# Kernel tuning notes

Hardware: AMD Instinct MI355X
Metric: run time of the kernel (lower is better)

The kernel has to match this reference:

```python
import jax, jax.numpy as jnp
import numpy as np
from jax import lax

FAULT_RATE = 0.1


def _quant_inject(key, x, num_faults):
    # scale/zero-point quantization to [0,255] (matches compute_scale_zero_point)
    mn, mx = x.min(), x.max()
    scale = (mx - mn) / 255.0
    zp = jnp.clip(-mn / scale, 0.0, 255.0)
    q = jnp.clip(jnp.round(zp + x / scale), 0.0, 255.0)
    if num_faults > 0:
        # vectorized equivalent of the serial fault loop: pick unique indices,
        # each consumes a random 1..8 fault budget; faulted bytes are zeroed
        # (the original loop sets tensor_bits = 0).
        n = q.size
        m = min(num_faults, n)  # each index consumes >= 1 fault
        k1, k2 = jax.random.split(key)
        cand = jax.random.permutation(k1, n)[:m]  # without replacement
        sizes = jax.random.randint(k2, (m,), 1, 9)
        prefix = jnp.cumsum(sizes) - sizes  # budget consumed before each pick
        keep = prefix < num_faults
        qf = q.reshape(-1)
        qf = qf.at[cand].set(jnp.where(keep, jnp.zeros((), q.dtype), qf[cand]))
        q = qf.reshape(q.shape)
    return scale * (q - zp)


def _conv(x, w, b):
    y = lax.conv_general_dilated(x, w, (1, 1), 'VALID',
                                 dimension_numbers=('NCHW', 'OIHW', 'NCHW'))
    return y + b[None, :, None, None]


def _maxpool(x):
    return lax.reduce_window(x, -np.inf, lax.max, (1, 1, 2, 2), (1, 1, 2, 2), 'VALID')


def _fault_schedule(total_activation_count):
    total_faults = int(total_activation_count * 8 * FAULT_RATE)
    rng = np.random.default_rng(0)
    return [int(v) for v in rng.multinomial(total_faults, np.ones(4) / 4)]


def _forward(x, conv1_w, conv1_b, conv2_w, conv2_b, fc_w, fc_b,
             fc1_w, fc1_b, fc2_w, fc2_b, fpl):
    ks = jax.random.split(jax.random.key(42), 11)
    x = _conv(x, conv1_w, conv1_b)
    x = _quant_inject(ks[0], x, 0)
    x = jax.nn.relu(x)
    x = _quant_inject(ks[1], x, fpl[0])
    x = _maxpool(x)
    x = _quant_inject(ks[2], x, 0)
    x = _conv(x, conv2_w, conv2_b)
    x = _quant_inject(ks[3], x, 0)
    x = jax.nn.relu(x)
    x = _quant_inject(ks[4], x, fpl[1])
    x = _maxpool(x)
    x = _quant_inject(ks[5], x, 0)
    x = x.reshape(x.shape[0], -1)  # [B, 400]
    x = x @ fc_w.T + fc_b
    x = _quant_inject(ks[6], x, 0)
    x = jax.nn.relu(x)
    x = _quant_inject(ks[7], x, fpl[2])
    x = x @ fc1_w.T + fc1_b
    x = _quant_inject(ks[8], x, 0)
    x = jax.nn.relu(x)
    x = _quant_inject(ks[9], x, fpl[3])
    x = x @ fc2_w.T + fc2_b
    x = _quant_inject(ks[10], x, 0)
    return jax.nn.log_softmax(x, axis=1)


def setup_inputs() -> dict:
    key = jax.random.key(0)
    ks = jax.random.split(key, 11)
    B = 8192
    return {
        'x': jax.random.normal(ks[0], (B, 1, 32, 32), jnp.float32),
        'conv1_w': jax.random.normal(ks[1], (6, 1, 5, 5), jnp.float32) * 0.2,
        'conv1_b': jax.random.normal(ks[2], (6,), jnp.float32) * 0.1,
        'conv2_w': jax.random.normal(ks[3], (16, 6, 5, 5), jnp.float32) * 0.08,
        'conv2_b': jax.random.normal(ks[4], (16,), jnp.float32) * 0.1,
        'fc_w': jax.random.normal(ks[5], (120, 400), jnp.float32) * 0.05,
        'fc_b': jax.random.normal(ks[6], (120,), jnp.float32) * 0.1,
        'fc1_w': jax.random.normal(ks[7], (84, 120), jnp.float32) * 0.09,
        'fc1_b': jax.random.normal(ks[8], (84,), jnp.float32) * 0.1,
        'fc2_w': jax.random.normal(ks[9], (10, 84), jnp.float32) * 0.1,
        'fc2_b': jax.random.normal(ks[10], (10,), jnp.float32) * 0.1,
        'total_activation_count': 833024,
    }


def reference(x, conv1_w, conv1_b, conv2_w, conv2_b, fc_w, fc_b,
              fc1_w, fc1_b, fc2_w, fc2_b, total_activation_count):
    fpl = _fault_schedule(total_activation_count)
    return _forward(x, conv1_w, conv1_b, conv2_w, conv2_b, fc_w, fc_b,
                    fc1_w, fc1_b, fc2_w, fc2_b, fpl)
```

## Files before the change

### kernel.cpp

```cpp
#include <hip/hip_runtime.h>
#include <cstdint>
#include <cstring>
#include <cmath>
#include <cstdlib>
#include <vector>
#include <thread>
#include <mutex>
#include <algorithm>

#define JAX_PARTITIONABLE 1


static inline uint32_t rotl32(uint32_t v, int d) { return (v << d) | (v >> (32 - d)); }

static inline void tf2x32(uint32_t k0, uint32_t k1, uint32_t c0, uint32_t c1,
                          uint32_t& o0, uint32_t& o1) {
  uint32_t ks0 = k0, ks1 = k1, ks2 = k0 ^ k1 ^ 0x1BD11BDAu;
  uint32_t ks[3] = {ks0, ks1, ks2};
  uint32_t x0 = c0 + ks0, x1 = c1 + ks1;
  static const int R[2][4] = {{13, 15, 26, 6}, {17, 29, 16, 24}};
  for (int g = 0; g < 5; g++) {
    const int* r = R[g & 1];
    for (int q = 0; q < 4; q++) { x0 += x1; x1 = rotl32(x1, r[q]); x1 ^= x0; }
    x0 += ks[(g + 1) % 3];
    x1 += ks[(g + 2) % 3] + (uint32_t)(g + 1);
  }
  o0 = x0; o1 = x1;
}

static void jax_split(const uint32_t key[2], int num, uint32_t (*out)[2]) {
#if JAX_PARTITIONABLE
  for (int i = 0; i < num; i++)
    tf2x32(key[0], key[1], 0u, (uint32_t)i, out[i][0], out[i][1]);
#else
  std::vector<uint32_t> o(2 * (size_t)num);
  for (int i = 0; i < num; i++) {
    uint32_t a, b;
    tf2x32(key[0], key[1], (uint32_t)i, (uint32_t)(num + i), a, b);
    o[i] = a; o[num + i] = b;
  }
  for (int i = 0; i < num; i++) { out[i][0] = o[2 * i]; out[i][1] = o[2 * i + 1]; }
#endif
}

static inline uint32_t jax_bits32_at(const uint32_t key[2], uint64_t n_total, uint64_t i) {
#if JAX_PARTITIONABLE
  uint32_t b0, b1;
  tf2x32(key[0], key[1], (uint32_t)(i >> 32), (uint32_t)i, b0, b1);
  return b0 ^ b1;
#else
  uint64_t half = (n_total + 1) / 2;
  uint64_t pi = (i < half) ? i : (i - half);
  uint32_t c1 = (half + pi < n_total) ? (uint32_t)(half + pi) : 0u;
  uint32_t b0, b1;
  tf2x32(key[0], key[1], (uint32_t)pi, c1, b0, b1);
  return (i < half) ? b0 : b1;
#endif
}

static void seedseq_zero_state(uint64_t out[4]) {
  const uint32_t INIT_A = 0x43b0d7e5u, MULT_A = 0x931e8875u;
  const uint32_t INIT_B = 0x8b51f9ddu, MULT_B = 0x58f38dedu;
  uint32_t pool[4];
  uint32_t hc = INIT_A;
  auto hashmix = [&](uint32_t v) -> uint32_t {
    v ^= hc; hc *= MULT_A; v *= hc; v ^= v >> 16; return v;
  };
  auto mixf = [](uint32_t x, uint32_t y) -> uint32_t {
    uint32_t r = x * 0xca01f9ddu - y * 0x4973f715u;
    r ^= r >> 16; return r;
  };
  uint32_t entropy0 = 0u;
  for (int i = 0; i < 4; i++) pool[i] = hashmix(i < 1 ? entropy0 : 0u);
  for (int s = 0; s < 4; s++)
    for (int d = 0; d < 4; d++)
      if (s != d) pool[d] = mixf(pool[d], hashmix(pool[s]));
  uint32_t st[8];
  uint32_t hc2 = INIT_B;
  int cyc = 0;
  for (int i = 0; i < 8; i++) {
    uint32_t v = pool[cyc]; cyc = (cyc + 1) & 3;
    v ^= hc2; hc2 *= MULT_B; v *= hc2; v ^= v >> 16;
    st[i] = v;
  }
  for (int k = 0; k < 4; k++)
    out[k] = (uint64_t)st[2 * k] | ((uint64_t)st[2 * k + 1] << 32);
}

struct PCG64 {
  __uint128_t state, inc;
  explicit PCG64(const uint64_t s[4]) {
    __uint128_t initstate = (((__uint128_t)s[0]) << 64) | s[1];
    __uint128_t initseq = (((__uint128_t)s[2]) << 64) | s[3];
    state = 0; inc = (initseq << 1) | 1;
    step(); state += initstate; step();
  }
  void step() {
    const __uint128_t MUL =
        (((__uint128_t)0x2360ed051fc65da4ULL) << 64) | 0x4385df649fccf645ULL;
    state = state * MUL + inc;
  }
  uint64_t next64() {
    step();
    uint64_t hi = (uint64_t)(state >> 64), lo = (uint64_t)state;
    uint64_t x = hi ^ lo;
    unsigned rot = (unsigned)(state >> 122);
    return (x >> rot) | (x << ((64u - rot) & 63u));
  }
  double nextd() { return (double)(next64() >> 11) * (1.0 / 9007199254740992.0); }
};

static int64_t binomial_inversion(PCG64& st, int64_t n, double p) {
  double q = 1.0 - p;
  double qn = std::exp(n * std::log(q));
  double np_ = n * p;
  int64_t bound = (int64_t)std::min((double)n, np_ + 10.0 * std::sqrt(np_ * q + 1));
  int64_t X = 0;
  double px = qn;
  double U = st.nextd();
  while (U > px) {
    X++;
    if (X > bound) { X = 0; px = qn; U = st.nextd(); }
    else { U -= px; px = ((n - X + 1) * p * px) / (X * q); }
  }
  return X;
}

static int64_t random_binomial_btpe(PCG64& st, int64_t n, double p) {
  double r, q, fm, p1, xm, xl, xr, c, laml, lamr, p2, p3, p4;
  double a, u, v, s, F, rho, t, A, nrq, x1, x2, f1, f2, z, z2, w, w2, x;
  int64_t m, y, k, i;
  r = std::min(p, 1.0 - p);
  q = 1.0 - r;
  fm = n * r + r;
  m = (int64_t)std::floor(fm);
  p1 = std::floor(2.195 * std::sqrt(n * r * q) - 4.6 * q) + 0.5;
  xm = m + 0.5;
  xl = xm - p1;
  xr = xm + p1;
  c = 0.134 + 20.5 / (15.3 + m);
  a = (fm - xl) / (fm - xl * r);
  laml = a * (1.0 + a / 2.0);
  a = (xr - fm) / (xr * q);
  lamr = a * (1.0 + a / 2.0);
  p2 = p1 * (1.0 + 2.0 * c);
  p3 = p2 + c / laml;
  p4 = p3 + c / lamr;

Step10:
  nrq = n * r * q;
  u = st.nextd() * p4;
  v = st.nextd();
  if (u > p1) goto Step20;
  y = (int64_t)std::floor(xm - p1 * v + u);
  goto Step60;
Step20:
  if (u > p2) goto Step30;
  x = xl + (u - p1) / c;
  v = v * c + 1.0 - std::fabs(m - x + 0.5) / p1;
  if (v > 1.0) goto Step10;
  y = (int64_t)std::floor(x);
  goto Step50;
Step30:
  if (u > p3) goto Step40;
  y = (int64_t)std::floor(xl + std::log(v) / laml);
  if ((y < 0) || (v == 0.0)) goto Step10;
  v = v * (u - p2) * laml;
  goto Step50;
Step40:
  y = (int64_t)std::floor(xr - std::log(v) / lamr);
  if ((y > n) || (v == 0.0)) goto Step10;
  v = v * (u - p3) * lamr;
  goto Step50;
Step50:
  k = (y > m) ? (y - m) : (m - y);
  if ((k > 20) && (k < (nrq / 2.0 - 1))) goto Step52;
  s = r / q;
  a = s * (n + 1);
  F = 1.0;
  if (m < y) { for (i = m + 1; i <= y; i++) F *= (a / i - s); }
  else if (m > y) { for (i = y + 1; i <= m; i++) F /= (a / i - s); }
  if (v > F) goto Step10;
  goto Step60;
Step52:
  rho = ((double)k / nrq) * ((k * (k / 3.0 + 0.625) + 0.16666666666666666) / nrq + 0.5);
  t = -((double)k) * k / (2 * nrq);
  A = std::log(v);
  if (A < (t - rho)) goto Step60;
  if (A > (t + rho)) goto Step10;
  x1 = (double)(y + 1);
  f1 = (double)(m + 1);
  z = (double)(n + 1 - m);
  w = (double)(n - y + 1);
  x2 = x1 * x1; f2 = f1 * f1; z2 = z * z; w2 = w * w;
  if (A > (xm * std::log(f1 / x1) + (n - m + 0.5) * std::log(z / w) +
           (y - m) * std::log(w * r / (x1 * q)) +
           (13680. - (462. - (132. - (99. - 140. / f2) / f2) / f2) / f2) / f1 / 166320. +
           (13680. - (462. - (132. - (99. - 140. / z2) / z2) / z2) / z2) / z / 166320. +
           (13680. - (462. - (132. - (99. - 140. / x2) / x2) / x2) / x2) / x1 / 166320. +
           (13680. - (462. - (132. - (99. - 140. / w2) / w2) / w2) / w2) / w / 166320.)) {
    goto Step10;
  }
Step60:
  if (p > 0.5) y = n - y;
  return y;
}

static int64_t random_binomial(PCG64& st, double p, int64_t n) {
  if (n == 0 || p == 0.0) return 0;
  if (p <= 0.5) {
    if (p * n <= 30.0) return binomial_inversion(st, n, p);
    return random_binomial_btpe(st, n, p);
  } else {
    double q = 1.0 - p;
    if (q * n <= 30.0) return n - binomial_inversion(st, n, q);
    return n - random_binomial_btpe(st, n, q);
  }
}

static void np_multinomial4(int64_t n, int64_t out[4]) {
  uint64_t ss[4];
  seedseq_zero_state(ss);
  PCG64 st(ss);
  double pix[4] = {0.25, 0.25, 0.25, 0.25};
  double remaining_p = 1.0;
  int64_t dn = n;
  out[0] = out[1] = out[2] = out[3] = 0;
  for (int j = 0; j < 3; j++) {
    out[j] = random_binomial(st, pix[j] / remaining_p, dn);
    dn -= out[j];
    if (dn <= 0) break;
    remaining_p -= pix[j];
  }
  if (dn > 0) out[3] = dn;
}

template <typename F>
static void pfor(size_t n, int T, const F& f) {
  if (n == 0) return;
  size_t chunk = (n + (size_t)T - 1) / (size_t)T;
  std::vector<std::thread> ths;
  for (int t = 0; t < T; t++) {
    size_t lo = (size_t)t * chunk;
    if (lo >= n) break;
    size_t hi = std::min(n, lo + chunk);
    ths.emplace_back([&f, lo, hi, t]() { f(lo, hi, t); });
  }
  for (auto& th : ths) th.join();
}

static void radix_pass16(const uint32_t* kin, const uint32_t* vin, uint32_t* kout,
                         uint32_t* vout, size_t n, int shift, int T,
                         std::vector<uint32_t>& hist) {
  const size_t BN = 65536;
  hist.assign((size_t)T * BN, 0u);
  pfor(n, T, [&](size_t lo, size_t hi, int t) {
    uint32_t* h = &hist[(size_t)t * BN];
    for (size_t i = lo; i < hi; i++) h[(kin[i] >> shift) & 0xFFFFu]++;
  });
  uint32_t sum = 0;
  for (size_t d = 0; d < BN; d++)
    for (int t = 0; t < T; t++) {
      uint32_t& hc = hist[(size_t)t * BN + d];
      uint32_t cnt = hc; hc = sum; sum += cnt;
    }
  pfor(n, T, [&](size_t lo, size_t hi, int t) {
    uint32_t* h = &hist[(size_t)t * BN];
    for (size_t i = lo; i < hi; i++) {
      uint32_t d = (kin[i] >> shift) & 0xFFFFu;
      uint32_t pos = h[d]++;
      kout[pos] = kin[i]; vout[pos] = vin[i];
    }
  });
}

static void shuffle_prefix(const uint32_t key[2], uint64_t n, uint32_t J,
                           uint32_t* out, int T) {
  if (J == 0) return;
  double nn = (double)(n < 1 ? 1 : n);
  int rounds = (int)std::ceil(3.0 * std::log(nn) / std::log(4294967295.0));
  size_t N = (size_t)n;
  std::vector<uint32_t> kbuf(N), vbuf(N), kt(N), vt(N);
  std::vector<uint32_t> hist;
  pfor(N, T, [&](size_t lo, size_t hi, int) {
    for (size_t i = lo; i < hi; i++) vbuf[i] = (uint32_t)i;
  });
  uint32_t cur[2] = {key[0], key[1]};
  for (int rd = 0; rd < rounds; rd++) {
    uint32_t ch[2][2];
    jax_split(cur, 2, ch);
    cur[0] = ch[0][0]; cur[1] = ch[0][1];
    uint32_t sk[2] = {ch[1][0], ch[1][1]};
#if JAX_PARTITIONABLE
    pfor(N, T, [&](size_t lo, size_t hi, int) {
      for (size_t i = lo; i < hi; i++) {
        uint32_t b0, b1;
        tf2x32(sk[0], sk[1], (uint32_t)(i >> 32), (uint32_t)i, b0, b1);
        kbuf[i] = b0 ^ b1;
      }
    });
#else
    {
      size_t half = (N + 1) / 2;
      pfor(half, T, [&](size_t lo, size_t hi, int) {
        for (size_t i = lo; i < hi; i++) {
          uint32_t c1v = (half + i < N) ? (uint32_t)(half + i) : 0u;
          uint32_t b0, b1;
          tf2x32(sk[0], sk[1], (uint32_t)i, c1v, b0, b1);
          kbuf[i] = b0;
          if (half + i < N) kbuf[half + i] = b1;
        }
      });
    }
#endif
    radix_pass16(kbuf.data(), vbuf.data(), kt.data(), vt.data(), N, 0, T, hist);
    radix_pass16(kt.data(), vt.data(), kbuf.data(), vbuf.data(), N, 16, T, hist);
  }
  for (uint32_t j = 0; j < J; j++) out[j] = vbuf[j];
  std::sort(out, out + J);
}


static uint32_t h_faults[4 * 65536];
static uint32_t h_blob[64 + 5 * 65536];
static int h_J[4] = {0, 0, 0, 0};
static int h_off[4] = {0, 0, 0, 0};
static int h_tot = 0;
static int h_nfw = 0;
static uint64_t h_tables_B = 0;

static void compute_fault_tables(uint64_t B, int Jout[4]) {
  int T = (int)std::thread::hardware_concurrency();
  if (T < 1) T = 1;
  if (T > 48) T = 48;
  int64_t fpl[4];
  np_multinomial4((int64_t)(833024ull * 8ull / 10ull), fpl);
  uint32_t k42[2] = {0u, 42u};
  uint32_t ks[11][2];
  jax_split(k42, 11, ks);
  const int kidx[4] = {1, 4, 7, 9};
  const uint64_t ns[4] = {B * 4704u, B * 1600u, B * 120u, B * 84u};
  for (int L = 0; L < 4; L++) {
    uint32_t ch[2][2];
    jax_split(ks[kidx[L]], 2, ch);
    uint32_t rc[2][2];
    jax_split(ch[1], 2, rc);
    int64_t nf = fpl[L];
    uint64_t m = ((uint64_t)nf < ns[L]) ? (uint64_t)nf : ns[L];
    int64_t csum = 0;
    uint32_t J = 0;
    for (uint64_t j = 0; j < m; j++) {
      if (csum >= nf) break;
      J++;
      csum += 1 + (int64_t)(jax_bits32_at(rc[1], m, j) & 7u);
    }
    if (J > 65536u) J = 65536u;
    shuffle_prefix(ch[0], ns[L], J, &h_faults[(size_t)L * 65536], T);
    Jout[L] = (int)J;
  }
  memset(h_blob, 0, 256);
  for (int s = 0; s < 11; s++) { h_blob[2 * s] = 0xFFFFFFFFu; h_blob[2 * s + 1] = 0u; }
  int tot = 0;
  for (int L = 0; L < 4; L++) {
    h_off[L] = tot;
    memcpy(h_blob + 64 + tot, h_faults + (size_t)L * 65536, (size_t)Jout[L] * 4);
    tot += Jout[L];
  }
  h_tot = tot;
  {
    std::vector<uint32_t> wv;
    wv.reserve(Jout[0]);
    for (int j = 0; j < Jout[0]; j++) {
      uint32_t e = h_faults[j];
      uint32_t im = e / 4704u, rem = e - im * 4704u;
      uint32_t c = rem / 784u, r2 = rem - c * 784u;
      uint32_t rr = r2 / 28u, cc = r2 - rr * 28u;
      wv.push_back(im * 1176u + c * 196u + (rr >> 1) * 14u + (cc >> 1));
    }
    std::sort(wv.begin(), wv.end());
    wv.erase(std::unique(wv.begin(), wv.end()), wv.end());
    h_nfw = (int)std::min<size_t>(wv.size(), 65536);
    memcpy(h_blob + 64 + tot, wv.data(), (size_t)h_nfw * 4);
  }
}

namespace {
struct FaultTableInit {
  FaultTableInit() {
    compute_fault_tables(8192ull, h_J);
    h_tables_B = 8192ull;
  }
};
FaultTableInit g_fault_table_init;
std::mutex g_table_mu;
}


#define INF_F __builtin_inff()

__device__ __forceinline__ uint32_t f_to_mono(float f) {
  uint32_t u = __float_as_uint(f);
  return (u & 0x80000000u) ? ~u : (u | 0x80000000u);
}
__device__ __forceinline__ float mono_to_f(uint32_t m) {
  uint32_t u = (m & 0x80000000u) ? (m & 0x7FFFFFFFu) : ~m;
  return __uint_as_float(u);
}

struct QP { float scale; float zp; };

__device__ __forceinline__ QP qp_make(float mn, float mx) {
  QP p;
  p.scale = (mx - mn) / 255.0f;
  p.zp = fminf(fmaxf((-mn) / p.scale, 0.0f), 255.0f);
  return p;
}
__device__ __forceinline__ QP qp_load(const uint32_t* stats, int s) {
  return qp_make(mono_to_f(stats[2 * s + 0]), mono_to_f(stats[2 * s + 1]));
}
__device__ __forceinline__ float quant_apply(float x, QP p) {
  float q = rintf(p.zp + x / p.scale);
  q = fminf(fmaxf(q, 0.0f), 255.0f);
  return p.scale * (q - p.zp);
}
__device__ __forceinline__ float quant_zero(QP p) { return p.scale * (0.0f - p.zp); }
__device__ __forceinline__ int q_idx(float x, QP p) {
  float q = rintf(p.zp + x / p.scale);
  q = fminf(fmaxf(q, 0.0f), 255.0f);
  return (int)q;
}

__device__ __forceinline__ QP qp_derive_relu(const uint32_t* stats, int s, QP qa) {
  float mn = mono_to_f(stats[2 * s + 0]);
  float mx = mono_to_f(stats[2 * s + 1]);
  float dmn = fmaxf(quant_apply(mn, qa), 0.0f);
  float dmx = fmaxf(quant_apply(mx, qa), 0.0f);
  return qp_make(dmn, dmx);
}

__device__ __forceinline__ void block_minmax(float lmn, float lmx, uint32_t* mn_slot,
                                             uint32_t* mx_slot) {
  for (int off = 32; off > 0; off >>= 1) {
    lmn = fminf(lmn, __shfl_down(lmn, off, 64));
    lmx = fmaxf(lmx, __shfl_down(lmx, off, 64));
  }
  __shared__ float wmn[16], wmx[16];
  int wid = threadIdx.x >> 6, lane = threadIdx.x & 63;
  int nw = (blockDim.x + 63) >> 6;
  if (lane == 0) { wmn[wid] = lmn; wmx[wid] = lmx; }
  __syncthreads();
  if (threadIdx.x == 0) {
    float m0 = wmn[0], m1 = wmx[0];
    for (int i = 1; i < nw; i++) { m0 = fminf(m0, wmn[i]); m1 = fmaxf(m1, wmx[i]); }
    atomicMin(mn_slot, f_to_mono(m0));
    atomicMax(mx_slot, f_to_mono(m1));
  }
}

__device__ __forceinline__ int lowb(const uint32_t* a, int n, uint32_t v) {
  int lo = 0, hi = n;
  while (lo < hi) {
    int mid = (lo + hi) >> 1;
    if (a[mid] < v) lo = mid + 1; else hi = mid;
  }
  return lo;
}


template <int IMG>
__device__ __forceinline__ void stage_img(const float* __restrict__ x, float* s_img,
                                          int ib0, int B) {
  for (int i = threadIdx.x; i < IMG * 256; i += 256) {
    int im = i >> 8, k = i & 255;
    if (ib0 + im < B) {
      float4 v = ((const float4*)(x + (size_t)(ib0 + im) * 1024))[k];
      int row = k >> 3, c4 = k & 7;
      ((float4*)s_img)[im * 320 + row * 10 + c4] = v;
    }
  }
}

__device__ __forceinline__ void stage_w1(const float* __restrict__ w, float* s_w) {
  if (threadIdx.x < 168) {
    int c = threadIdx.x / 28, f = threadIdx.x - c * 28;
    s_w[threadIdx.x] = (f < 25) ? w[c * 25 + f] : 0.0f;
  }
}

template <int O>
__device__ __forceinline__ void conv1_rowpair(const float* __restrict__ img, int r0,
                                              int colbase, const float* wr,
                                              float acc0[14], float acc1[14]) {
#pragma unroll
  for (int ir = 0; ir < 6; ir++) {
    float f[20];
    const float* rp = img + (r0 + ir) * 40 + colbase;
#pragma unroll
    for (int k = 0; k < 5; k++) *(float4*)&f[4 * k] = *(const float4*)&rp[4 * k];
    if (ir < 5) {
#pragma unroll
      for (int j = 0; j < 5; j++)
#pragma unroll
        for (int cc = 0; cc < 14; cc++)
          acc0[cc] = fmaf(f[O + cc + j], wr[ir * 5 + j], acc0[cc]);
    }
    if (ir >= 1) {
#pragma unroll
      for (int j = 0; j < 5; j++)
#pragma unroll
        for (int cc = 0; cc < 14; cc++)
          acc1[cc] = fmaf(f[O + cc + j], wr[(ir - 1) * 5 + j], acc1[cc]);
    }
  }
}

__global__ __launch_bounds__(256) void k_conv1_mat(const float* __restrict__ x,
    const float* __restrict__ w, const float* __restrict__ b,
    float* __restrict__ wmax, float* __restrict__ side,
    const uint32_t* __restrict__ fw, int nfw_g,
    uint32_t* __restrict__ stats, int B) {
  __shared__ __align__(16) float s_img[4 * 1280];
  __shared__ __align__(16) float s_w[168];
  __shared__ float s_b[8];
  __shared__ uint32_t s_fw[64];
  __shared__ int s_flo, s_fn;
  int ib0 = blockIdx.x * 4;
  stage_img<4>(x, s_img, ib0, B);
  stage_w1(w, s_w);
  if (threadIdx.x < 6) s_b[threadIdx.x] = b[threadIdx.x];
  if (threadIdx.x == 0) {
    uint32_t w0 = (uint32_t)ib0 * 1176u;
    uint32_t w1 = (uint32_t)(ib0 + 4) * 1176u;
    int lo = lowb(fw, nfw_g, w0);
    s_flo = lo; s_fn = lowb(fw, nfw_g, w1) - lo;
  }
  __syncthreads();
  int fn = s_fn, flo = s_flo;
  for (int i = threadIdx.x; i < fn && i < 64; i += 256) s_fw[i] = fw[flo + i];
  __syncthreads();
  const uint32_t* fwa = (fn <= 64) ? s_fw : (fw + flo);

  float lmn = INF_F, lmx = -INF_F;
#pragma unroll 1
  for (int task = threadIdx.x; task < 4 * 168; task += 256) {
    int im = task / 168, rem = task - im * 168;
    if (ib0 + im >= B) continue;
    int c = rem / 28, r2 = rem - c * 28, pr = r2 >> 1, h = r2 & 1;
    float wr[25];
#pragma unroll
    for (int k = 0; k < 25; k++) wr[k] = s_w[c * 28 + k];
    float bias = s_b[c];
    float acc0[14], acc1[14];
#pragma unroll
    for (int cc = 0; cc < 14; cc++) { acc0[cc] = bias; acc1[cc] = bias; }
    const float* img = &s_img[im * 1280];
    if (h == 0) conv1_rowpair<0>(img, 2 * pr, 0, wr, acc0, acc1);
    else        conv1_rowpair<2>(img, 2 * pr, 12, wr, acc0, acc1);
    uint32_t wid0 = (uint32_t)(ib0 + im) * 1176u + (uint32_t)(c * 196 + pr * 14 + h * 7);
    float* dst = wmax + wid0;
#pragma unroll
    for (int k = 0; k < 7; k++) {
      float wm = fmaxf(fmaxf(acc0[2 * k], acc0[2 * k + 1]),
                       fmaxf(acc1[2 * k], acc1[2 * k + 1]));
      dst[k] = wm;
    }
    if (fn > 0) {
      int a = lowb(fwa, fn, wid0);
      while (a < fn) {
        uint32_t wg = fwa[a];
        if (wg >= wid0 + 7u) break;
#pragma unroll
        for (int k = 0; k < 7; k++) {
          if ((int)(wg - wid0) == k) {
            float4 sv;
            sv.x = acc0[2 * k]; sv.y = acc0[2 * k + 1];
            sv.z = acc1[2 * k]; sv.w = acc1[2 * k + 1];
            *(float4*)&side[4 * (flo + a)] = sv;
          }
        }
        a++;
      }
    }
#pragma unroll
    for (int cc = 0; cc < 14; cc++) {
      lmn = fminf(lmn, fminf(acc0[cc], acc1[cc]));
      lmx = fmaxf(lmx, fmaxf(acc0[cc], acc1[cc]));
    }
  }
  block_minmax(lmn, lmx, &stats[0], &stats[1]);
}

__global__ __launch_bounds__(256) void k_pool1(const float* __restrict__ wmax,
    const float* __restrict__ side, const uint32_t* __restrict__ fw, int nfw_g,
    const uint32_t* __restrict__ faults, int J,
    uint32_t* __restrict__ stats, float* __restrict__ p1, int B) {
  __shared__ float s_V[256];
  __shared__ uint32_t s_fw[64], s_fl[64];
  __shared__ int s_wlo, s_wn, s_elo, s_en;
  QP q0 = qp_load(stats, 0);
  QP qB = qp_derive_relu(stats, 0, q0);
  {
    int i = threadIdx.x;
    float a = fmaxf(q0.scale * ((float)i - q0.zp), 0.0f);
    float kq = fminf(fmaxf(rintf(qB.zp + a / qB.scale), 0.0f), 255.0f);
    s_V[i] = qB.scale * (kq - qB.zp);
  }
  int T0 = blockIdx.x * 256;
  if (threadIdx.x == 0) {
    int im0 = T0 / 84, imL = (T0 + 255) / 84;
    uint32_t w0 = (uint32_t)im0 * 1176u, w1 = (uint32_t)(imL + 1) * 1176u;
    int lo = lowb(fw, nfw_g, w0);
    s_wlo = lo; s_wn = lowb(fw, nfw_g, w1) - lo;
    uint32_t e0 = (uint32_t)im0 * 4704u, e1 = (uint32_t)(imL + 1) * 4704u;
    int lo2 = lowb(faults, J, e0);
    s_elo = lo2; s_en = lowb(faults, J, e1) - lo2;
  }
  __syncthreads();
  int wn = s_wn, wlo = s_wlo, en = s_en, elo = s_elo;
  for (int i = threadIdx.x; i < wn && i < 64; i += 256) s_fw[i] = fw[wlo + i];
  for (int i = threadIdx.x; i < en && i < 64; i += 256) s_fl[i] = faults[elo + i];
  __syncthreads();
  const uint32_t* fwa = (wn <= 64) ? s_fw : (fw + wlo);
  const uint32_t* fla = (en <= 64) ? s_fl : (faults + elo);

  float lmn = INF_F, lmx = -INF_F;
  int T = T0 + threadIdx.x;
  if (T < B * 84) {
    int im = T / 84, rem = T - im * 84;
    int c = rem / 14, pr = rem - c * 14;
    uint32_t rb = (uint32_t)im * 1176u + (uint32_t)(c * 196 + pr * 14);
    const float* src = wmax + rb;
    float v[14];
#pragma unroll
    for (int q = 0; q < 7; q++) {
      float2 wm = *(const float2*)&src[2 * q];
      v[2 * q]     = s_V[q_idx(wm.x, q0)];
      v[2 * q + 1] = s_V[q_idx(wm.y, q0)];
    }
    if (wn > 0) {
      int a = lowb(fwa, wn, rb);
      while (a < wn) {
        uint32_t wg = fwa[a];
        if (wg >= rb + 14u) break;
        int wc = (int)(wg - rb);
        float4 sv = *(const float4*)&side[4 * (wlo + a)];
        uint32_t eb = (uint32_t)im * 4704u + (uint32_t)(c * 784 + 2 * pr * 28 + 2 * wc);
        float m0, mm = 0.0f;
        int p2_;
        p2_ = lowb(fla, en, eb);       m0 = (p2_ < en && fla[p2_] == eb)       ? 0.0f : (float)q_idx(sv.x, q0);
        mm = fmaxf(mm * 0.0f, m0);
        p2_ = lowb(fla, en, eb + 1u);  m0 = (p2_ < en && fla[p2_] == eb + 1u)  ? 0.0f : (float)q_idx(sv.y, q0);
        mm = fmaxf(mm, m0);
        p2_ = lowb(fla, en, eb + 28u); m0 = (p2_ < en && fla[p2_] == eb + 28u) ? 0.0f : (float)q_idx(sv.z, q0);
        mm = fmaxf(mm, m0);
        p2_ = lowb(fla, en, eb + 29u); m0 = (p2_ < en && fla[p2_] == eb + 29u) ? 0.0f : (float)q_idx(sv.w, q0);
        mm = fmaxf(mm, m0);
        float aa = fmaxf(q0.scale * (mm - q0.zp), 0.0f);
        float kq = fminf(fmaxf(rintf(qB.zp + aa / qB.scale), 0.0f), 255.0f);
#pragma unroll
        for (int k = 0; k < 14; k++) if (k == wc) v[k] = qB.scale * (kq - qB.zp);
        a++;
      }
    }
    float* dst = p1 + rb;
#pragma unroll
    for (int q = 0; q < 7; q++) {
      float2 o; o.x = v[2 * q]; o.y = v[2 * q + 1];
      *(float2*)&dst[2 * q] = o;
      lmn = fminf(lmn, fminf(o.x, o.y));
      lmx = fmaxf(lmx, fmaxf(o.x, o.y));
    }
  }
  block_minmax(lmn, lmx, &stats[4], &stats[5]);
}

__global__ __launch_bounds__(256) void k_conv2(const float* __restrict__ p1,
    const float* __restrict__ w, const float* __restrict__ b,
    float* __restrict__ raw, uint32_t* __restrict__ stats, int B) {
  __shared__ __align__(16) float s_in[8 * 1680];
  __shared__ __align__(16) float s_w[16 * 6 * 28];
  __shared__ float s_b[16];
  int ib0 = blockIdx.x * 8;
  QP q2 = qp_load(stats, 2);
  for (int i = threadIdx.x; i < 8 * 1176; i += 256) {
    int im = i / 1176, rem = i - im * 1176;
    if (ib0 + im < B) {
      int ci = rem / 196, r2 = rem - ci * 196;
      int rr = r2 / 14, cc = r2 - rr * 14;
      float v = quant_apply(p1[(size_t)(ib0 + im) * 1176 + rem], q2);
      s_in[im * 1680 + ci * 280 + rr * 20 + cc] = v;
    }
  }
  for (int i = threadIdx.x; i < 2688; i += 256) {
    int fi = i / 28, f = i - fi * 28;
    s_w[i] = (f < 25) ? w[fi * 25 + f] : 0.0f;
  }
  if (threadIdx.x < 16) s_b[threadIdx.x] = b[threadIdx.x];
  __syncthreads();
  float lmn = INF_F, lmx = -INF_F;
#pragma unroll 1
  for (int task = threadIdx.x; task < 640; task += 256) {
    int im = task / 80, rem = task - im * 80;
    if (ib0 + im >= B) continue;
    int c2p = rem / 10, r = rem - c2p * 10;
    int cA = 2 * c2p, cB = 2 * c2p + 1;
    float accA[10], accB[10];
    float bA = s_b[cA], bB = s_b[cB];
#pragma unroll
    for (int cc = 0; cc < 10; cc++) { accA[cc] = bA; accB[cc] = bB; }
    const float* inb = &s_in[im * 1680];
#pragma unroll 1
    for (int ci = 0; ci < 6; ci++) {
      float wrA[28], wrB[28];
#pragma unroll
      for (int k = 0; k < 7; k++) {
        *(float4*)&wrA[4 * k] = *(const float4*)&s_w[(cA * 6 + ci) * 28 + 4 * k];
        *(float4*)&wrB[4 * k] = *(const float4*)&s_w[(cB * 6 + ci) * 28 + 4 * k];
      }
      const float* cb = inb + ci * 280;
#pragma unroll
      for (int i = 0; i < 5; i++) {
        float f[16];
        const float* rp = cb + (r + i) * 20;
#pragma unroll
        for (int k = 0; k < 4; k++) *(float4*)&f[4 * k] = *(const float4*)&rp[4 * k];
#pragma unroll
        for (int j = 0; j < 5; j++) {
#pragma unroll
          for (int cc = 0; cc < 10; cc++) accA[cc] = fmaf(f[cc + j], wrA[i * 5 + j], accA[cc]);
#pragma unroll
          for (int cc = 0; cc < 10; cc++) accB[cc] = fmaf(f[cc + j], wrB[i * 5 + j], accB[cc]);
        }
      }
    }
    float* rbA = raw + (size_t)(ib0 + im) * 1600 + cA * 100 + r * 10;
    float* rbB = raw + (size_t)(ib0 + im) * 1600 + cB * 100 + r * 10;
#pragma unroll
    for (int cc = 0; cc < 10; cc++) {
      rbA[cc] = accA[cc]; rbB[cc] = accB[cc];
      lmn = fminf(lmn, fminf(accA[cc], accB[cc]));
      lmx = fmaxf(lmx, fmaxf(accA[cc], accB[cc]));
    }
  }
  block_minmax(lmn, lmx, &stats[6], &stats[7]);
}

__global__ __launch_bounds__(256) void k_pool2s(const float* __restrict__ raw,
    uint32_t* __restrict__ stats, const uint32_t* __restrict__ faults, int J,
    float* __restrict__ p2, int B) {
  __shared__ float s_K[256];
  __shared__ uint32_t s_fl[64];
  __shared__ int s_lo, s_nf;
  QP q3 = qp_load(stats, 3);
  QP qE = qp_derive_relu(stats, 3, q3);
  {
    int i = threadIdx.x;
    float a = fmaxf(q3.scale * ((float)i - q3.zp), 0.0f);
    float kq = rintf(qE.zp + a / qE.scale);
    s_K[i] = fminf(fmaxf(kq, 0.0f), 255.0f);
  }
  int T0 = blockIdx.x * 256;
  if (threadIdx.x == 0) {
    int im0 = T0 / 80;
    int imL = (T0 + 255) / 80;
    uint32_t lo32 = (uint32_t)im0 * 1600u;
    uint32_t hi32 = (uint32_t)(imL + 1) * 1600u;
    int lo = lowb(faults, J, lo32);
    s_lo = lo; s_nf = lowb(faults, J, hi32) - lo;
  }
  __syncthreads();
  int nf = s_nf, flo = s_lo;
  for (int i = threadIdx.x; i < nf && i < 64; i += 256) s_fl[i] = faults[flo + i];
  __syncthreads();
  const uint32_t* farr = (nf <= 64) ? s_fl : (faults + flo);

  float lmn = INF_F, lmx = -INF_F;
  int T = T0 + threadIdx.x;
  if (T < B * 80) {
    int im = T / 80, rem = T - im * 80;
    int c = rem / 5, pr = rem - c * 5;
    uint32_t e0 = (uint32_t)im * 1600u + (uint32_t)(c * 100 + 2 * pr * 10);
    const float* src = raw + (size_t)im * 1600 + c * 100 + (2 * pr) * 10;
    float kk[20];
#pragma unroll
    for (int q = 0; q < 5; q++) {
      float4 v = *(const float4*)&src[4 * q];
      kk[4 * q + 0] = s_K[q_idx(v.x, q3)];
      kk[4 * q + 1] = s_K[q_idx(v.y, q3)];
      kk[4 * q + 2] = s_K[q_idx(v.z, q3)];
      kk[4 * q + 3] = s_K[q_idx(v.w, q3)];
    }
    if (nf > 0) {
      int a = lowb(farr, nf, e0);
      while (a < nf) {
        uint32_t g = farr[a];
        if (g >= e0 + 20u) break;
        int d = (int)(g - e0);
#pragma unroll
        for (int cc = 0; cc < 20; cc++) if (cc == d) kk[cc] = 0.0f;
        a++;
      }
    }
    float* dst = p2 + (size_t)im * 400 + c * 25 + pr * 5;
#pragma unroll
    for (int q = 0; q < 5; q++) {
      float kp = fmaxf(fmaxf(kk[2 * q], kk[2 * q + 1]),
                       fmaxf(kk[10 + 2 * q], kk[10 + 2 * q + 1]));
      float v = qE.scale * (kp - qE.zp);
      dst[q] = v;
      lmn = fminf(lmn, v); lmx = fmaxf(lmx, v);
    }
  }
  block_minmax(lmn, lmx, &stats[10], &stats[11]);
}

template <int IN, int OUT, int ROWS, int SPLIT, bool CHAIN>
__global__ __launch_bounds__(256) void k_fc(const float* __restrict__ in,
    const float* __restrict__ w, const float* __restrict__ bias,
    float* __restrict__ out, uint32_t* stats, int squant, int s_out,
    const uint32_t* __restrict__ faults, int J) {
  __shared__ __align__(16) float rows[ROWS * IN];
  int b0 = blockIdx.x * ROWS;
  QP p{1.0f, 0.0f};
  if (CHAIN) {
    QP qa = qp_load(stats, squant);
    p = qp_derive_relu(stats, squant, qa);
    for (int i = threadIdx.x; i < ROWS * IN; i += 256)
      rows[i] = quant_apply(fmaxf(quant_apply(in[(size_t)b0 * IN + i], qa), 0.0f), p);
  } else {
    p = qp_load(stats, squant);
    for (int i = threadIdx.x; i < ROWS * IN; i += 256)
      rows[i] = quant_apply(in[(size_t)b0 * IN + i], p);
  }
  if (faults) {
    __syncthreads();
    uint32_t base = (uint32_t)b0 * IN;
    int lo = lowb(faults, J, base), hi2 = lowb(faults, J, base + ROWS * IN);
    float qz = quant_zero(p);
    for (int t = lo + (int)threadIdx.x; t < hi2; t += 256) rows[faults[t] - base] = qz;
  }
  __syncthreads();
  constexpr int RP = ROWS / SPLIT;
  int o = threadIdx.x % OUT;
  int sp = threadIdx.x / OUT;
  float lmn = INF_F, lmx = -INF_F;
  if (sp < SPLIT) {
    float acc[RP];
#pragma unroll
    for (int r = 0; r < RP; r++) acc[r] = bias[o];
    const float* wr = &w[(size_t)o * IN];
    for (int k = 0; k < IN; k += 4) {
      float4 wv = *(const float4*)&wr[k];
#pragma unroll
      for (int r = 0; r < RP; r++) {
        float4 xv = *(const float4*)&rows[(sp * RP + r) * IN + k];
        acc[r] = fmaf(xv.x, wv.x, acc[r]);
        acc[r] = fmaf(xv.y, wv.y, acc[r]);
        acc[r] = fmaf(xv.z, wv.z, acc[r]);
        acc[r] = fmaf(xv.w, wv.w, acc[r]);
      }
    }
#pragma unroll
    for (int r = 0; r < RP; r++) {
      out[(size_t)(b0 + sp * RP + r) * OUT + o] = acc[r];
      lmn = fminf(lmn, acc[r]); lmx = fmaxf(lmx, acc[r]);
    }
  }
  block_minmax(lmn, lmx, &stats[2 * s_out], &stats[2 * s_out + 1]);
}

__global__ __launch_bounds__(256) void k_logsoftmax(const float* __restrict__ logits,
    float* __restrict__ out, const uint32_t* stats, int slot, int B) {
  int i = blockIdx.x * 256 + threadIdx.x;
  if (i >= B) return;
  QP p = qp_load(stats, slot);
  float v[10];
  float m = -INF_F;
#pragma unroll
  for (int k = 0; k < 10; k++) {
    v[k] = quant_apply(logits[(size_t)i * 10 + k], p);
    m = fmaxf(m, v[k]);
  }
  float s = 0.0f;
#pragma unroll
  for (int k = 0; k < 10; k++) s += expf(v[k] - m);
  float ls = logf(s);
#pragma unroll
  for (int k = 0; k < 10; k++) out[(size_t)i * 10 + k] = (v[k] - m) - ls;
}

extern "C" void kernel_launch(void* const* d_in, const int* in_sizes, int n_in,
                              void* d_out, int out_size, void* d_ws, size_t ws_size,
                              hipStream_t stream) {
  const float* x    = (const float*)d_in[0];
  const float* c1w  = (const float*)d_in[1];
  const float* c1b  = (const float*)d_in[2];
  const float* c2w  = (const float*)d_in[3];
  const float* c2b  = (const float*)d_in[4];
  const float* fcw  = (const float*)d_in[5];
  const float* fcb  = (const float*)d_in[6];
  const float* fc1w = (const float*)d_in[7];
  const float* fc1b = (const float*)d_in[8];
  const float* fc2w = (const float*)d_in[9];
  const float* fc2b = (const float*)d_in[10];
  float* out = (float*)d_out;
  const int B = in_sizes[0] / 1024;

  if ((uint64_t)B != h_tables_B) {
    std::lock_guard<std::mutex> lk(g_table_mu);
    if ((uint64_t)B != h_tables_B) {
      compute_fault_tables((uint64_t)B, h_J);
      h_tables_B = (uint64_t)B;
    }
  }

  uint8_t* ws = (uint8_t*)d_ws;
  uint32_t* stats = (uint32_t*)ws;
  uint32_t* fl = (uint32_t*)(ws + 256);
  size_t off = 256 + (size_t)5 * 65536 * sizeof(uint32_t);
  float* p1   = (float*)(ws + off); off += (size_t)B * 1176 * 4;
  float* p2   = (float*)(ws + off); off += (size_t)B * 400 * 4;
  float* h1   = (float*)(ws + off); off += (size_t)B * 120 * 4;
  float* h2   = (float*)(ws + off); off += (size_t)B * 84 * 4;
  float* lg   = (float*)(ws + off); off += (size_t)B * 10 * 4;
  float* raw2 = (float*)(ws + off); off += (size_t)B * 1600 * 4;
  float* wmax = (float*)(ws + off); off += (size_t)B * 1176 * 4;
  float* side = (float*)(ws + off); off += (size_t)65536 * 16;
  if (ws_size < off) return;

  const uint32_t* f0 = fl + h_off[0];
  const uint32_t* f1 = fl + h_off[1];
  const uint32_t* f2 = fl + h_off[2];
  const uint32_t* f3 = fl + h_off[3];
  const uint32_t* fw = fl + h_tot;

  hipMemcpyAsync(ws, h_blob, 256 + (size_t)(h_tot + h_nfw) * sizeof(uint32_t),
                 hipMemcpyHostToDevice, stream);

  int g4 = (B + 3) / 4, g8 = (B + 7) / 8;

  k_conv1_mat<<<g4, 256, 0, stream>>>(x, c1w, c1b, wmax, side, fw, h_nfw, stats, B);
  k_pool1<<<(B * 84 + 255) / 256, 256, 0, stream>>>(wmax, side, fw, h_nfw,
                                                    f0, h_J[0], stats, p1, B);

  k_conv2<<<g8, 256, 0, stream>>>(p1, c2w, c2b, raw2, stats, B);
  k_pool2s<<<(B * 80 + 255) / 256, 256, 0, stream>>>(raw2, stats, f1, h_J[1], p2, B);

  k_fc<400, 120, 16, 2, false><<<B / 16, 256, 0, stream>>>(p2, fcw, fcb, h1, stats,
                                                           5, 6, nullptr, 0);
  k_fc<120, 84, 16, 2, true><<<B / 16, 256, 0, stream>>>(h1, fc1w, fc1b, h2, stats,
                                                         6, 8, f2, h_J[2]);
  k_fc<84, 10, 32, 8, true><<<B / 32, 256, 0, stream>>>(h2, fc2w, fc2b, lg, stats,
                                                        8, 10, f3, h_J[3]);
  k_logsoftmax<<<(B + 255) / 256, 256, 0, stream>>>(lg, out, stats, 10, B);
}
```

Before: 623.4 us.

## Swizzle conv1 shared image, remap conv2 tasks by channel pair, pin host blob

Conv1 now stores the staged image in shared memory with a padded, XOR-like swizzled row stride so the float4 row reads hit fewer bank conflicts, at the cost of more LDS per block. Conv2 gives each warp a fixed output-channel pair and has each thread handle up to three (image,row) tasks, so the weights are loaded once per input channel instead of once per task. This raises register pressure by tripling the accumulators. The host fault blob is page-locked so its upload can use faster DMA.

```diff
diff --git a/kernel.cpp b/kernel.cpp
--- a/kernel.cpp
+++ b/kernel.cpp
@@ -389,6 +389,7 @@
   FaultTableInit() {
     compute_fault_tables(8192ull, h_J);
     h_tables_B = 8192ull;
+    (void)hipHostRegister(h_blob, sizeof(h_blob), hipHostRegisterDefault);
   }
 };
 FaultTableInit g_fault_table_init;
@@ -467,6 +468,8 @@
 }
 
 
+__device__ __forceinline__ int sw4(int r) { return ((r >> 1) & 7) << 2; }
+
 template <int IMG>
 __device__ __forceinline__ void stage_img(const float* __restrict__ x, float* s_img,
                                           int ib0, int B) {
@@ -475,7 +478,7 @@
     if (ib0 + im < B) {
       float4 v = ((const float4*)(x + (size_t)(ib0 + im) * 1024))[k];
       int row = k >> 3, c4 = k & 7;
-      ((float4*)s_img)[im * 320 + row * 10 + c4] = v;
+      ((float4*)s_img)[im * 512 + row * 16 + ((row >> 1) & 7) + c4] = v;
     }
   }
 }
@@ -493,8 +496,9 @@
                                               float acc0[14], float acc1[14]) {
 #pragma unroll
   for (int ir = 0; ir < 6; ir++) {
+    int r = r0 + ir;
     float f[20];
-    const float* rp = img + (r0 + ir) * 40 + colbase;
+    const float* rp = img + r * 64 + sw4(r) + colbase;
 #pragma unroll
     for (int k = 0; k < 5; k++) *(float4*)&f[4 * k] = *(const float4*)&rp[4 * k];
     if (ir < 5) {
@@ -519,7 +523,7 @@
     float* __restrict__ wmax, float* __restrict__ side,
     const uint32_t* __restrict__ fw, int nfw_g,
     uint32_t* __restrict__ stats, int B) {
-  __shared__ __align__(16) float s_img[4 * 1280];
+  __shared__ __align__(16) float s_img[4 * 2048];
   __shared__ __align__(16) float s_w[168];
   __shared__ float s_b[8];
   __shared__ uint32_t s_fw[64];
@@ -553,7 +557,7 @@
     float acc0[14], acc1[14];
 #pragma unroll
     for (int cc = 0; cc < 14; cc++) { acc0[cc] = bias; acc1[cc] = bias; }
-    const float* img = &s_img[im * 1280];
+    const float* img = &s_img[im * 2048];
     if (h == 0) conv1_rowpair<0>(img, 2 * pr, 0, wr, acc0, acc1);
     else        conv1_rowpair<2>(img, 2 * pr, 12, wr, acc0, acc1);
     uint32_t wid0 = (uint32_t)(ib0 + im) * 1176u + (uint32_t)(c * 196 + pr * 14 + h * 7);
@@ -697,27 +701,33 @@
   }
   if (threadIdx.x < 16) s_b[threadIdx.x] = b[threadIdx.x];
   __syncthreads();
-  float lmn = INF_F, lmx = -INF_F;
+
+  int c2p = threadIdx.x >> 5;
+  int sub = threadIdx.x & 31;
+  int cA = 2 * c2p, cB = cA + 1;
+  int tt0 = sub, tt1 = sub + 32, tt2 = sub + 64;
+  float accA[3][10], accB[3][10];
+  float bA = s_b[cA], bB = s_b[cB];
+#pragma unroll
+  for (int t = 0; t < 3; t++)
+#pragma unroll
+    for (int cc = 0; cc < 10; cc++) { accA[t][cc] = bA; accB[t][cc] = bB; }
+
 #pragma unroll 1
-  for (int task = threadIdx.x; task < 640; task += 256) {
-    int im = task / 80, rem = task - im * 80;
-    if (ib0 + im >= B) continue;
-    int c2p = rem / 10, r = rem - c2p * 10;
-    int cA = 2 * c2p, cB = 2 * c2p + 1;
-    float accA[10], accB[10];
-    float bA = s_b[cA], bB = s_b[cB];
-#pragma unroll
-    for (int cc = 0; cc < 10; cc++) { accA[cc] = bA; accB[cc] = bB; }
-    const float* inb = &s_in[im * 1680];
-#pragma unroll 1
-    for (int ci = 0; ci < 6; ci++) {
-      float wrA[28], wrB[28];
-#pragma unroll
-      for (int k = 0; k < 7; k++) {
-        *(float4*)&wrA[4 * k] = *(const float4*)&s_w[(cA * 6 + ci) * 28 + 4 * k];
-        *(float4*)&wrB[4 * k] = *(const float4*)&s_w[(cB * 6 + ci) * 28 + 4 * k];
-      }
-      const float* cb = inb + ci * 280;
+  for (int ci = 0; ci < 6; ci++) {
+    float wrA[28], wrB[28];
+#pragma unroll
+    for (int k = 0; k < 7; k++) {
+      *(float4*)&wrA[4 * k] = *(const float4*)&s_w[(cA * 6 + ci) * 28 + 4 * k];
+      *(float4*)&wrB[4 * k] = *(const float4*)&s_w[(cB * 6 + ci) * 28 + 4 * k];
+    }
+#pragma unroll
+    for (int t = 0; t < 3; t++) {
+      int task = (t == 0) ? tt0 : (t == 1) ? tt1 : tt2;
+      if (task >= 80) continue;
+      int im = task / 10, r = task - im * 10;
+      if (ib0 + im >= B) continue;
+      const float* cb = &s_in[im * 1680 + ci * 280];
 #pragma unroll
       for (int i = 0; i < 5; i++) {
         float f[16];
@@ -727,19 +737,30 @@
 #pragma unroll
         for (int j = 0; j < 5; j++) {
 #pragma unroll
-          for (int cc = 0; cc < 10; cc++) accA[cc] = fmaf(f[cc + j], wrA[i * 5 + j], accA[cc]);
-#pragma unroll
-          for (int cc = 0; cc < 10; cc++) accB[cc] = fmaf(f[cc + j], wrB[i * 5 + j], accB[cc]);
+          for (int cc = 0; cc < 10; cc++)
+            accA[t][cc] = fmaf(f[cc + j], wrA[i * 5 + j], accA[t][cc]);
+#pragma unroll
+          for (int cc = 0; cc < 10; cc++)
+            accB[t][cc] = fmaf(f[cc + j], wrB[i * 5 + j], accB[t][cc]);
         }
       }
     }
+  }
+
+  float lmn = INF_F, lmx = -INF_F;
+#pragma unroll
+  for (int t = 0; t < 3; t++) {
+    int task = (t == 0) ? tt0 : (t == 1) ? tt1 : tt2;
+    if (task >= 80) continue;
+    int im = task / 10, r = task - im * 10;
+    if (ib0 + im >= B) continue;
     float* rbA = raw + (size_t)(ib0 + im) * 1600 + cA * 100 + r * 10;
     float* rbB = raw + (size_t)(ib0 + im) * 1600 + cB * 100 + r * 10;
 #pragma unroll
     for (int cc = 0; cc < 10; cc++) {
-      rbA[cc] = accA[cc]; rbB[cc] = accB[cc];
-      lmn = fminf(lmn, fminf(accA[cc], accB[cc]));
-      lmx = fmaxf(lmx, fmaxf(accA[cc], accB[cc]));
+      rbA[cc] = accA[t][cc]; rbB[cc] = accB[t][cc];
+      lmn = fminf(lmn, fminf(accA[t][cc], accB[t][cc]));
+      lmx = fmaxf(lmx, fmaxf(accA[t][cc], accB[t][cc]));
     }
   }
   block_minmax(lmn, lmx, &stats[6], &stats[7]);
```

New measurement: 532.6 us. -14.6%, faster.
